# Performance work log

Measured on AMD Instinct MI355X. Metric: run time of the kernel, lower is better.

Reference implementation:

```python
import jax, jax.numpy as jnp
import numpy as np

N_NODES = 100000
N_EDGES = 1600000
IN_DIM, HID, N_CLS = 128, 256, 40


def setup_inputs() -> dict:
    key = jax.random.key(0)
    ks = jax.random.split(key, 8)
    x = jax.random.normal(ks[0], (N_NODES, IN_DIM), dtype=jnp.float32)
    edge_index = jax.random.randint(ks[1], (2, N_EDGES), 0, N_NODES, dtype=jnp.int64)
    def glorot(k, shape):
        scale = (6.0 / (shape[0] + shape[1])) ** 0.5
        return jax.random.uniform(k, shape, jnp.float32, -scale, scale)
    return {
        "x": x,
        "edge_index": edge_index,
        "W1": glorot(ks[2], (IN_DIM, HID)),
        "b1": jnp.zeros((HID,), jnp.float32),
        "W2": glorot(ks[3], (HID, HID)),
        "b2": jnp.zeros((HID,), jnp.float32),
        "W3": glorot(ks[4], (HID, N_CLS)),
        "b3": jnp.zeros((N_CLS,), jnp.float32),
    }


def _gcn_norm(edge_index, num_nodes):
    # Add self-loops, then symmetric normalization deg^-1/2 * deg^-1/2 (PyG GCNConv).
    loops = jnp.arange(num_nodes, dtype=edge_index.dtype)
    src = jnp.concatenate([edge_index[0], loops])
    dst = jnp.concatenate([edge_index[1], loops])
    deg = jax.ops.segment_sum(jnp.ones_like(dst, dtype=jnp.float32), dst,
                              num_segments=num_nodes)
    dinv = jnp.where(deg > 0, jax.lax.rsqrt(deg), 0.0)
    norm = dinv[src] * dinv[dst]  # [E + N]
    return src, dst, norm


def _gcn_conv(x, W, b, src, dst, norm, num_nodes):
    h = x @ W                       # [N, out] dense GEMM first (out <= in here is fine)
    msg = h[src] * norm[:, None]    # irregular gather, [E+N, out]
    out = jax.ops.segment_sum(msg, dst, num_segments=num_nodes)  # scatter-add
    return out + b


def reference(x, edge_index, W1, b1, W2, b2, W3, b3):
    n = x.shape[0]
    src, dst, norm = _gcn_norm(edge_index, n)
    h = jax.nn.relu(_gcn_conv(x, W1, b1, src, dst, norm, n))
    h = jax.nn.relu(_gcn_conv(h, W2, b2, src, dst, norm, n))
    h = _gcn_conv(h, W3, b3, src, dst, norm, n)
    return jax.nn.log_softmax(h, axis=1)
```

## Files before the change

kernel.cpp:

```cpp
#include <hip/hip_runtime.h>
#include <stdint.h>
#include <math.h>

#define N_NODES 100000
#define N_EDGES 1600000
#define IN_DIM 128
#define HID 256
#define N_CLS 40
#define NBKT 391
#define NPB 391

typedef __attribute__((ext_vector_type(8))) short short8;
typedef __attribute__((ext_vector_type(4))) float f32x4;

__device__ __forceinline__ unsigned short f2bf(float f) {
  unsigned b = __float_as_uint(f);
  b += 0x7fffu + ((b >> 16) & 1u);
  return (unsigned short)(b >> 16);
}
__device__ __forceinline__ float bflo(unsigned u) { return __uint_as_float(u << 16); }
__device__ __forceinline__ float bfhi(unsigned u) { return __uint_as_float(u & 0xffff0000u); }

__device__ __forceinline__ int load_idx(const void* eidx, int flag, size_t pos) {
  return flag ? (int)((const long long*)eidx)[pos] : ((const int*)eidx)[pos];
}

__global__ __launch_bounds__(512) void k_pre0(const unsigned int* __restrict__ ew,
                                              int* __restrict__ flag,
                                              int* __restrict__ hist) {
  int t = threadIdx.x;
  for (int k = t; k < NBKT; k += 512) hist[k] = 0;
  __shared__ unsigned int sh[512];
  unsigned int v = 0;
  for (int k = t; k < 4096; k += 512) v |= ew[2 * k + 1];
  sh[t] = v;
  __syncthreads();
  for (int s = 256; s > 0; s >>= 1) {
    if (t < s) sh[t] |= sh[t + s];
    __syncthreads();
  }
  if (t == 0) flag[0] = (sh[0] == 0u) ? 1 : 0;
}

__global__ __launch_bounds__(256) void k_hist(const void* __restrict__ eidx,
                                              const int* __restrict__ flagp,
                                              int* __restrict__ hist) {
  __shared__ int lh[NBKT];
  int t = threadIdx.x;
  for (int k = t; k < NBKT; k += 256) lh[k] = 0;
  __syncthreads();
  int flag = flagp[0];
  int base = blockIdx.x * 4096;
#pragma unroll
  for (int j = 0; j < 16; j++) {
    int e = base + j * 256 + t;
    if (e < N_EDGES) {
      int d = load_idx(eidx, flag, (size_t)N_EDGES + e);
      atomicAdd(&lh[d >> 8], 1);
    }
  }
  __syncthreads();
  for (int k = t; k < NBKT; k += 256) {
    int c = lh[k];
    if (c) atomicAdd(&hist[k], c);
  }
}

__global__ __launch_bounds__(512) void k_bscan(const int* __restrict__ hist,
                                               int* __restrict__ bucket_start,
                                               int* __restrict__ bucket_cursor) {
  __shared__ int sh[512];
  int t = threadIdx.x;
  int v = (t < NBKT) ? hist[t] : 0;
  sh[t] = v;
  __syncthreads();
  for (int off = 1; off < 512; off <<= 1) {
    int u = (t >= off) ? sh[t - off] : 0;
    __syncthreads();
    sh[t] += u;
    __syncthreads();
  }
  if (t < NBKT) {
    bucket_start[t + 1] = sh[t];
    bucket_cursor[t] = sh[t] - v;
  }
  if (t == 0) bucket_start[0] = 0;
}

__global__ __launch_bounds__(256) void k_part(const void* __restrict__ eidx,
                                              const int* __restrict__ flagp,
                                              int* __restrict__ bucket_cursor,
                                              uint2* __restrict__ bpairs) {
  __shared__ int lcur[NBKT];
  int t = threadIdx.x;
  for (int k = t; k < NBKT; k += 256) lcur[k] = 0;
  __syncthreads();
  int flag = flagp[0];
  int base = blockIdx.x * 4096;
#pragma unroll
  for (int j = 0; j < 16; j++) {
    int e = base + j * 256 + t;
    if (e < N_EDGES) {
      int d = load_idx(eidx, flag, (size_t)N_EDGES + e);
      atomicAdd(&lcur[d >> 8], 1);
    }
  }
  __syncthreads();
  for (int k = t; k < NBKT; k += 256) {
    int c = lcur[k];
    int g = c ? atomicAdd(&bucket_cursor[k], c) : 0;
    lcur[k] = g;
  }
  __syncthreads();
#pragma unroll
  for (int j = 0; j < 16; j++) {
    int e = base + j * 256 + t;
    if (e < N_EDGES) {
      int s = load_idx(eidx, flag, e);
      int d = load_idx(eidx, flag, (size_t)N_EDGES + e);
      int p = atomicAdd(&lcur[d >> 8], 1);
      bpairs[p] = make_uint2((unsigned)s, (unsigned)d);
    }
  }
}

__global__ __launch_bounds__(256) void k_bsort(const uint2* __restrict__ bpairs,
                                               const int* __restrict__ bucket_start,
                                               int* __restrict__ row_start,
                                               float* __restrict__ dinv,
                                               int* __restrict__ csr_src) {
  __shared__ int ldeg[256], lsum[256], lcur[256];
  int b = blockIdx.x, t = threadIdx.x;
  int d0 = b << 8;
  int nd = min(256, N_NODES - d0);
  int base = bucket_start[b];
  int n = bucket_start[b + 1] - base;
  ldeg[t] = 0;
  __syncthreads();
  for (int i = t; i < n; i += 256) {
    uint2 p = bpairs[base + i];
    atomicAdd(&ldeg[p.y - d0], 1);
  }
  __syncthreads();
  lsum[t] = ldeg[t];
  __syncthreads();
  for (int off = 1; off < 256; off <<= 1) {
    int v = (t >= off) ? lsum[t - off] : 0;
    __syncthreads();
    lsum[t] += v;
    __syncthreads();
  }
  int excl = lsum[t] - ldeg[t];
  if (t < nd) {
    row_start[d0 + t] = base + excl;
    dinv[d0 + t] = rsqrtf((float)(ldeg[t] + 1));
  }
  lcur[t] = base + excl;
  __syncthreads();
  for (int i = t; i < n; i += 256) {
    uint2 p = bpairs[base + i];
    int pos = atomicAdd(&lcur[p.y - d0], 1);
    csr_src[pos] = (int)p.x;
  }
  if (b == 0 && t == 0) row_start[N_NODES] = N_EDGES;
}

__global__ __launch_bounds__(256) void k_wprep(const float* __restrict__ W1,
                                               const float* __restrict__ W2,
                                               const float* __restrict__ W3,
                                               unsigned short* __restrict__ T1,
                                               unsigned short* __restrict__ T2,
                                               unsigned short* __restrict__ T3) {
  int idx = blockIdx.x * 256 + threadIdx.x;
  if (idx < 32768) {
    int n = idx >> 7, k = idx & 127;
    T1[idx] = f2bf(W1[(size_t)k * HID + n]);
  } else if (idx < 98304) {
    int j = idx - 32768;
    int n = j >> 8, k = j & 255;
    T2[j] = f2bf(W2[(size_t)k * HID + n]);
  } else if (idx < 131072) {
    int j = idx - 98304;
    int n = j >> 8, k = j & 255;
    T3[j] = f2bf((n < N_CLS) ? W3[(size_t)k * N_CLS + n] : 0.f);
  }
}

__global__ __launch_bounds__(256) void k_qx(const float* __restrict__ x,
                                            const float* __restrict__ dinv,
                                            unsigned short* __restrict__ xq,
                                            float* __restrict__ sw_x) {
  int node = (blockIdx.x << 2) + (threadIdx.x >> 6);
  int lane = threadIdx.x & 63;
  if (node >= N_NODES) return;
  float2 v = ((const float2*)x)[(size_t)node * 64 + lane];
  float m = fmaxf(fabsf(v.x), fabsf(v.y));
  for (int off = 32; off; off >>= 1) m = fmaxf(m, __shfl_down(m, off));
  m = __shfl(m, 0);
  float inv = (m > 0.f) ? 127.f / m : 0.f;
  int q0 = __float2int_rn(v.x * inv);
  int q1 = __float2int_rn(v.y * inv);
  xq[(size_t)node * 64 + lane] = (unsigned short)((q0 & 0xff) | ((q1 & 0xff) << 8));
  if (lane == 0) sw_x[node] = dinv[node] * ((m > 0.f) ? m / 127.f : 0.f);
}

__device__ __forceinline__ void up4u(unsigned v, float w,
                                     float& a0, float& a1, float& a2, float& a3) {
  a0 = fmaf((float)(v & 0xffu), w, a0);
  a1 = fmaf((float)((v >> 8) & 0xffu), w, a1);
  a2 = fmaf((float)((v >> 16) & 0xffu), w, a2);
  a3 = fmaf((float)(v >> 24), w, a3);
}

__global__ __launch_bounds__(256) void k_agg256i(const unsigned* __restrict__ tbl,
                                                 uint2* __restrict__ out,
                                                 const float* __restrict__ dinv,
                                                 const float* __restrict__ sw2,
                                                 const int* __restrict__ row_start,
                                                 const int* __restrict__ csr_src) {
  int node = (blockIdx.x << 2) + (threadIdx.x >> 6);
  int lane = threadIdx.x & 63;
  if (node >= N_NODES) return;
  const unsigned* col = tbl + lane;
  const float* sw = sw2 + ((lane >= 32) ? N_NODES : 0);
  float d = dinv[node];
  float ws = sw[node];
  unsigned v0 = col[(size_t)node * 64];
  float a0 = 0.f, a1 = 0.f, a2 = 0.f, a3 = 0.f;
  up4u(v0, ws, a0, a1, a2, a3);
  int e = row_start[node], e1 = row_start[node + 1];
  for (; e + 8 <= e1; e += 8) {
    int i0 = csr_src[e],     i1 = csr_src[e + 1], i2 = csr_src[e + 2], i3 = csr_src[e + 3];
    int i4 = csr_src[e + 4], i5 = csr_src[e + 5], i6 = csr_src[e + 6], i7 = csr_src[e + 7];
    float w0 = sw[i0], w1 = sw[i1], w2 = sw[i2], w3 = sw[i3];
    float w4 = sw[i4], w5 = sw[i5], w6 = sw[i6], w7 = sw[i7];
    unsigned r0 = col[(size_t)i0 * 64], r1 = col[(size_t)i1 * 64];
    unsigned r2 = col[(size_t)i2 * 64], r3 = col[(size_t)i3 * 64];
    unsigned r4 = col[(size_t)i4 * 64], r5 = col[(size_t)i5 * 64];
    unsigned r6 = col[(size_t)i6 * 64], r7 = col[(size_t)i7 * 64];
    up4u(r0, w0, a0, a1, a2, a3);
    up4u(r1, w1, a0, a1, a2, a3);
    up4u(r2, w2, a0, a1, a2, a3);
    up4u(r3, w3, a0, a1, a2, a3);
    up4u(r4, w4, a0, a1, a2, a3);
    up4u(r5, w5, a0, a1, a2, a3);
    up4u(r6, w6, a0, a1, a2, a3);
    up4u(r7, w7, a0, a1, a2, a3);
  }
  for (; e < e1; e++) {
    int i0 = csr_src[e];
    float w0 = sw[i0];
    unsigned r0 = col[(size_t)i0 * 64];
    up4u(r0, w0, a0, a1, a2, a3);
  }
  a0 *= d; a1 *= d; a2 *= d; a3 *= d;
  uint2 o;
  o.x = f2bf(a0) | ((unsigned)f2bf(a1) << 16);
  o.y = f2bf(a2) | ((unsigned)f2bf(a3) << 16);
  out[(size_t)node * 64 + lane] = o;
}

__global__ __launch_bounds__(256) void k_agg128i(const unsigned short* __restrict__ tbl,
                                                 unsigned* __restrict__ out,
                                                 const float* __restrict__ dinv,
                                                 const float* __restrict__ sw,
                                                 const int* __restrict__ row_start,
                                                 const int* __restrict__ csr_src) {
  int node = (blockIdx.x << 2) + (threadIdx.x >> 6);
  int lane = threadIdx.x & 63;
  if (node >= N_NODES) return;
  const unsigned short* col = tbl + lane;
  float d = dinv[node];
  float ws = sw[node];
  unsigned short v0 = col[(size_t)node * 64];
  float a0 = (float)(signed char)(v0 & 0xff) * ws;
  float a1 = (float)(signed char)(v0 >> 8) * ws;
  int e = row_start[node], e1 = row_start[node + 1];
  for (; e + 8 <= e1; e += 8) {
    int i0 = csr_src[e],     i1 = csr_src[e + 1], i2 = csr_src[e + 2], i3 = csr_src[e + 3];
    int i4 = csr_src[e + 4], i5 = csr_src[e + 5], i6 = csr_src[e + 6], i7 = csr_src[e + 7];
    float w0 = sw[i0], w1 = sw[i1], w2 = sw[i2], w3 = sw[i3];
    float w4 = sw[i4], w5 = sw[i5], w6 = sw[i6], w7 = sw[i7];
    unsigned short r0 = col[(size_t)i0 * 64], r1 = col[(size_t)i1 * 64];
    unsigned short r2 = col[(size_t)i2 * 64], r3 = col[(size_t)i3 * 64];
    unsigned short r4 = col[(size_t)i4 * 64], r5 = col[(size_t)i5 * 64];
    unsigned short r6 = col[(size_t)i6 * 64], r7 = col[(size_t)i7 * 64];
    a0 = fmaf((float)(signed char)(r0 & 0xff), w0, a0);
    a1 = fmaf((float)(signed char)(r0 >> 8), w0, a1);
    a0 = fmaf((float)(signed char)(r1 & 0xff), w1, a0);
    a1 = fmaf((float)(signed char)(r1 >> 8), w1, a1);
    a0 = fmaf((float)(signed char)(r2 & 0xff), w2, a0);
    a1 = fmaf((float)(signed char)(r2 >> 8), w2, a1);
    a0 = fmaf((float)(signed char)(r3 & 0xff), w3, a0);
    a1 = fmaf((float)(signed char)(r3 >> 8), w3, a1);
    a0 = fmaf((float)(signed char)(r4 & 0xff), w4, a0);
    a1 = fmaf((float)(signed char)(r4 >> 8), w4, a1);
    a0 = fmaf((float)(signed char)(r5 & 0xff), w5, a0);
    a1 = fmaf((float)(signed char)(r5 >> 8), w5, a1);
    a0 = fmaf((float)(signed char)(r6 & 0xff), w6, a0);
    a1 = fmaf((float)(signed char)(r6 >> 8), w6, a1);
    a0 = fmaf((float)(signed char)(r7 & 0xff), w7, a0);
    a1 = fmaf((float)(signed char)(r7 >> 8), w7, a1);
  }
  for (; e < e1; e++) {
    int i0 = csr_src[e];
    float w0 = sw[i0];
    unsigned short r0 = col[(size_t)i0 * 64];
    a0 = fmaf((float)(signed char)(r0 & 0xff), w0, a0);
    a1 = fmaf((float)(signed char)(r0 >> 8), w0, a1);
  }
  a0 *= d; a1 *= d;
  out[(size_t)node * 64 + lane] = f2bf(a0) | ((unsigned)f2bf(a1) << 16);
}

__global__ __launch_bounds__(256) void k_gemm_mfma(const unsigned short* __restrict__ A,
                                                   int lda,
                                                   const unsigned short* __restrict__ B,
                                                   const float* __restrict__ bias,
                                                   unsigned short* __restrict__ C, int ldc,
                                                   int M, int K, int relu) {
  __shared__ alignas(16) unsigned short As[128][40];
  __shared__ alignas(16) unsigned short Bs[128][40];
  int tid = threadIdx.x;
  int lane = tid & 63, wv = tid >> 6;
  int wy = wv >> 1, wx = wv & 1;
  int row0 = blockIdx.x * 128, col0 = blockIdx.y * 128;

  f32x4 acc[4][4];
#pragma unroll
  for (int i = 0; i < 4; i++)
#pragma unroll
    for (int j = 0; j < 4; j++) acc[i][j] = 0.f;

  int sr0 = tid >> 2;
  int sc = (tid & 3) * 8;

  for (int k0 = 0; k0 < K; k0 += 32) {
#pragma unroll
    for (int it = 0; it < 2; it++) {
      int r = sr0 + it * 64;
      int gr = row0 + r;
      short8 va = 0;
      if (gr < M) va = *(const short8*)(A + (size_t)gr * lda + k0 + sc);
      *(short8*)&As[r][sc] = va;
      short8 vb = *(const short8*)(B + (size_t)(col0 + r) * K + k0 + sc);
      *(short8*)&Bs[r][sc] = vb;
    }
    __syncthreads();

    int ar = wy * 64 + (lane & 15);
    int br = wx * 64 + (lane & 15);
    int kk = (lane >> 4) * 8;
    short8 a[4], b[4];
#pragma unroll
    for (int mi = 0; mi < 4; mi++) a[mi] = *(const short8*)&As[ar + mi * 16][kk];
#pragma unroll
    for (int ni = 0; ni < 4; ni++) b[ni] = *(const short8*)&Bs[br + ni * 16][kk];
#pragma unroll
    for (int mi = 0; mi < 4; mi++)
#pragma unroll
      for (int ni = 0; ni < 4; ni++)
        acc[mi][ni] = __builtin_amdgcn_mfma_f32_16x16x32_bf16(a[mi], b[ni], acc[mi][ni], 0, 0, 0);
    __syncthreads();
  }

  int mbase = row0 + wy * 64;
  int nbase = col0 + wx * 64;
#pragma unroll
  for (int ni = 0; ni < 4; ni++) {
    int gc = nbase + ni * 16 + (lane & 15);
    if (gc >= ldc) continue;
    float bz = bias ? bias[gc] : 0.f;
#pragma unroll
    for (int mi = 0; mi < 4; mi++) {
      f32x4 v = acc[mi][ni];
#pragma unroll
      for (int r = 0; r < 4; r++) {
        int gr = mbase + mi * 16 + (lane >> 4) * 4 + r;
        if (gr < M) {
          float o = v[r] + bz;
          if (relu) o = fmaxf(o, 0.f);
          C[(size_t)gr * ldc + gc] = f2bf(o);
        }
      }
    }
  }
}

__global__ __launch_bounds__(256) void k_gemm_q(const unsigned short* __restrict__ A,
                                                int lda,
                                                const unsigned short* __restrict__ B,
                                                const float* __restrict__ bias,
                                                const float* __restrict__ dinv,
                                                unsigned* __restrict__ hq,
                                                float* __restrict__ sw_h,
                                                int M, int K) {
  __shared__ alignas(16) unsigned short As[128][40];
  __shared__ alignas(16) unsigned short Bs[128][40];
  __shared__ float rmax[128][2];
  __shared__ float rscale[128];
  __shared__ alignas(16) unsigned char qtile[128][128];
  int tid = threadIdx.x;
  int lane = tid & 63, wv = tid >> 6;
  int wy = wv >> 1, wx = wv & 1;
  int quad = lane >> 4;
  int row0 = blockIdx.x * 128, col0 = blockIdx.y * 128;
  int half = blockIdx.y;

  f32x4 acc[4][4];
#pragma unroll
  for (int i = 0; i < 4; i++)
#pragma unroll
    for (int j = 0; j < 4; j++) acc[i][j] = 0.f;

  int sr0 = tid >> 2;
  int sc = (tid & 3) * 8;

  for (int k0 = 0; k0 < K; k0 += 32) {
#pragma unroll
    for (int it = 0; it < 2; it++) {
      int r = sr0 + it * 64;
      int gr = row0 + r;
      short8 va = 0;
      if (gr < M) va = *(const short8*)(A + (size_t)gr * lda + k0 + sc);
      *(short8*)&As[r][sc] = va;
      short8 vb = *(const short8*)(B + (size_t)(col0 + r) * K + k0 + sc);
      *(short8*)&Bs[r][sc] = vb;
    }
    __syncthreads();

    int ar = wy * 64 + (lane & 15);
    int br = wx * 64 + (lane & 15);
    int kk = quad * 8;
    short8 a[4], b[4];
#pragma unroll
    for (int mi = 0; mi < 4; mi++) a[mi] = *(const short8*)&As[ar + mi * 16][kk];
#pragma unroll
    for (int ni = 0; ni < 4; ni++) b[ni] = *(const short8*)&Bs[br + ni * 16][kk];
#pragma unroll
    for (int mi = 0; mi < 4; mi++)
#pragma unroll
      for (int ni = 0; ni < 4; ni++)
        acc[mi][ni] = __builtin_amdgcn_mfma_f32_16x16x32_bf16(a[mi], b[ni], acc[mi][ni], 0, 0, 0);
    __syncthreads();
  }

#pragma unroll
  for (int ni = 0; ni < 4; ni++) {
    int gc = col0 + wx * 64 + ni * 16 + (lane & 15);
    float bz = bias[gc];
#pragma unroll
    for (int mi = 0; mi < 4; mi++)
#pragma unroll
      for (int r = 0; r < 4; r++)
        acc[mi][ni][r] = fmaxf(acc[mi][ni][r] + bz, 0.f);
  }
  float m16[4][4];
#pragma unroll
  for (int mi = 0; mi < 4; mi++)
#pragma unroll
    for (int r = 0; r < 4; r++)
      m16[mi][r] = fmaxf(fmaxf(acc[mi][0][r], acc[mi][1][r]),
                         fmaxf(acc[mi][2][r], acc[mi][3][r]));
#pragma unroll
  for (int st = 1; st < 16; st <<= 1)
#pragma unroll
    for (int mi = 0; mi < 4; mi++)
#pragma unroll
      for (int r = 0; r < 4; r++)
        m16[mi][r] = fmaxf(m16[mi][r], __shfl_xor(m16[mi][r], st));
  {
    int i = lane & 15;
    int row = wy * 64 + (i >> 2) * 16 + quad * 4 + (i & 3);
    rmax[row][wx] = m16[i >> 2][i & 3];
  }
  __syncthreads();
  if (tid < 128) {
    float mx = fmaxf(rmax[tid][0], rmax[tid][1]);
    rscale[tid] = (mx > 0.f) ? 255.f / mx : 0.f;
    int grow = row0 + tid;
    if (grow < M) sw_h[half * N_NODES + grow] = dinv[grow] * ((mx > 0.f) ? mx / 255.f : 0.f);
  }
  __syncthreads();
#pragma unroll
  for (int ni = 0; ni < 4; ni++) {
    int c = wx * 64 + ni * 16 + (lane & 15);
#pragma unroll
    for (int mi = 0; mi < 4; mi++)
#pragma unroll
      for (int r = 0; r < 4; r++) {
        int row = wy * 64 + mi * 16 + quad * 4 + r;
        qtile[row][c] = (unsigned char)__float2uint_rn(acc[mi][ni][r] * rscale[row]);
      }
  }
  __syncthreads();
  const uint4* qt = (const uint4*)qtile;
#pragma unroll
  for (int k = 0; k < 4; k++) {
    int idx = tid + k * 256;
    int row = idx >> 3, p = idx & 7;
    int grow = row0 + row;
    if (grow < M)
      *(uint4*)(hq + (size_t)grow * 64 + half * 32 + p * 4) = qt[idx];
  }
}

__global__ __launch_bounds__(256) void k_agg40_lsm(const unsigned* __restrict__ in,
                                                   float* __restrict__ out,
                                                   const float* __restrict__ dinv,
                                                   const int* __restrict__ row_start,
                                                   const int* __restrict__ csr_src,
                                                   const float* __restrict__ bias) {
  int node = (blockIdx.x << 2) + (threadIdx.x >> 6);
  int lane = threadIdx.x & 63;
  if (node >= N_NODES) return;
  int g = (lane >= 40) ? 2 : (lane >= 20 ? 1 : 0);
  int c = lane - g * 20;
  bool act3 = lane < 60;
  const unsigned* base = in + c;
  float d = dinv[node];
  float ws = (g == 0 && act3) ? d : 0.f;
  unsigned u0 = base[(size_t)node * 32];
  float a0 = bflo(u0) * ws, a1 = bfhi(u0) * ws;
  int e1 = row_start[node + 1];
  int eb = row_start[node];
  for (; eb + 12 <= e1; eb += 12) {
    int ea = eb + g, eb2 = eb + 3 + g, ec = eb + 6 + g, ed = eb + 9 + g;
    int ia = csr_src[ea], ib = csr_src[eb2], ic = csr_src[ec], id = csr_src[ed];
    float wa = act3 ? dinv[ia] : 0.f;
    float wb = act3 ? dinv[ib] : 0.f;
    float wc = act3 ? dinv[ic] : 0.f;
    float wd = act3 ? dinv[id] : 0.f;
    unsigned ra = base[(size_t)ia * 32];
    unsigned rb = base[(size_t)ib * 32];
    unsigned rc = base[(size_t)ic * 32];
    unsigned rd = base[(size_t)id * 32];
    a0 = fmaf(bflo(ra), wa, a0); a1 = fmaf(bfhi(ra), wa, a1);
    a0 = fmaf(bflo(rb), wb, a0); a1 = fmaf(bfhi(rb), wb, a1);
    a0 = fmaf(bflo(rc), wc, a0); a1 = fmaf(bfhi(rc), wc, a1);
    a0 = fmaf(bflo(rd), wd, a0); a1 = fmaf(bfhi(rd), wd, a1);
  }
  for (; eb < e1; eb += 3) {
    int ea = eb + g;
    bool v = act3 && (ea < e1);
    int ia = v ? csr_src[ea] : 0;
    float wa = v ? dinv[ia] : 0.f;
    unsigned ra = base[(size_t)ia * 32];
    a0 = fmaf(bflo(ra), wa, a0); a1 = fmaf(bfhi(ra), wa, a1);
  }
  a0 += __shfl(a0, c + 20) + __shfl(a0, c + 40);
  a1 += __shfl(a1, c + 20) + __shfl(a1, c + 40);
  bool act = lane < 20;
  float v0 = act ? a0 * d + bias[2 * lane] : -INFINITY;
  float v1 = act ? a1 * d + bias[2 * lane + 1] : -INFINITY;
  float m = fmaxf(v0, v1);
  for (int off = 32; off; off >>= 1) m = fmaxf(m, __shfl_down(m, off));
  m = __shfl(m, 0);
  float s = act ? expf(v0 - m) + expf(v1 - m) : 0.f;
  for (int off = 32; off; off >>= 1) s += __shfl_down(s, off);
  s = __shfl(s, 0);
  float lse = m + logf(s);
  if (act) {
    out[(size_t)node * N_CLS + 2 * lane] = v0 - lse;
    out[(size_t)node * N_CLS + 2 * lane + 1] = v1 - lse;
  }
}

extern "C" void kernel_launch(void* const* d_in, const int* in_sizes, int n_in,
                              void* d_out, int out_size, void* d_ws, size_t ws_size,
                              hipStream_t stream) {
  const float* x  = (const float*)d_in[0];
  const void*  ei = d_in[1];
  const float* W1 = (const float*)d_in[2];
  const float* b1 = (const float*)d_in[3];
  const float* W2 = (const float*)d_in[4];
  const float* b2 = (const float*)d_in[5];
  const float* W3 = (const float*)d_in[6];
  const float* b3 = (const float*)d_in[7];
  float* out = (float*)d_out;

  char* w = (char*)d_ws;
  auto alloc = [&](size_t bytes) {
    char* p = w;
    w += (bytes + 255) & ~(size_t)255;
    return p;
  };
  int*   flag          = (int*)alloc(64);
  int*   hist          = (int*)alloc((size_t)NBKT * 4);
  int*   bucket_start  = (int*)alloc((size_t)(NBKT + 1) * 4);
  int*   bucket_cursor = (int*)alloc((size_t)NBKT * 4);
  uint2* bpairs        = (uint2*)alloc((size_t)N_EDGES * 8);
  int*   csr_src       = (int*)alloc((size_t)N_EDGES * 4);
  int*   row_start     = (int*)alloc(((size_t)N_NODES + 1) * 4);
  float* dinv          = (float*)alloc((size_t)N_NODES * 4);
  float* sw_x          = (float*)alloc((size_t)N_NODES * 4);
  float* sw_h          = (float*)alloc((size_t)N_NODES * 2 * 4);
  unsigned short* Wt1  = (unsigned short*)alloc((size_t)HID * IN_DIM * 2);
  unsigned short* Wt2  = (unsigned short*)alloc((size_t)HID * HID * 2);
  unsigned short* Wt3  = (unsigned short*)alloc((size_t)128 * HID * 2);
  unsigned short* xq   = (unsigned short*)alloc((size_t)N_NODES * 64 * 2);
  unsigned*       hq   = (unsigned*)alloc((size_t)N_NODES * 64 * 4);
  char* R0 = alloc((size_t)N_NODES * HID * 2);
  char* R1 = alloc((size_t)N_NODES * HID * 2);

  unsigned*       aggX  = (unsigned*)R0;
  uint2*          aggH1 = (uint2*)R0;
  unsigned short* h2    = (unsigned short*)R1;
  unsigned short* C3    = (unsigned short*)R0;

  const int nb_w1 = (N_NODES + 3) / 4;
  const int gm    = (N_NODES + 127) / 128;

  k_pre0<<<1, 512, 0, stream>>>((const unsigned int*)ei, flag, hist);
  k_hist<<<NPB, 256, 0, stream>>>(ei, flag, hist);
  k_bscan<<<1, 512, 0, stream>>>(hist, bucket_start, bucket_cursor);
  k_part<<<NPB, 256, 0, stream>>>(ei, flag, bucket_cursor, bpairs);
  k_bsort<<<NBKT, 256, 0, stream>>>(bpairs, bucket_start, row_start, dinv, csr_src);

  k_wprep<<<512, 256, 0, stream>>>(W1, W2, W3, Wt1, Wt2, Wt3);
  k_qx<<<nb_w1, 256, 0, stream>>>(x, dinv, xq, sw_x);

  k_agg128i<<<nb_w1, 256, 0, stream>>>(xq, aggX, dinv, sw_x, row_start, csr_src);
  k_gemm_q<<<dim3(gm, 2), 256, 0, stream>>>((const unsigned short*)aggX, IN_DIM, Wt1, b1,
                                            dinv, hq, sw_h, N_NODES, IN_DIM);
  k_agg256i<<<nb_w1, 256, 0, stream>>>(hq, aggH1, dinv, sw_h, row_start, csr_src);
  k_gemm_mfma<<<dim3(gm, 2), 256, 0, stream>>>((const unsigned short*)aggH1, HID, Wt2, b2,
                                               h2, HID, N_NODES, HID, 1);
  k_gemm_mfma<<<dim3(gm, 1), 256, 0, stream>>>(h2, HID, Wt3, nullptr,
                                               C3, 64, N_NODES, HID, 0);
  k_agg40_lsm<<<nb_w1, 256, 0, stream>>>((const unsigned*)C3, out, dinv, row_start,
                                         csr_src, b3);
}
```

Measured before the change: 525.0 us.

## Prefetch scalarized CSR indices and interleave per-half scale weights in aggregation kernels

Both aggregation kernels now make node and row bounds wave-uniform with readfirstlane. Each loads the next eight neighbor indices as scalars one iteration ahead, and handles the remainder with a padded masked batch of eight instead of a scalar tail loop. The per-node scale array for the 256-wide layer is stored interleaved (node*2+half) instead of as two separate halves, so both halves of a wave read adjacent words. The aim is to cut vector index loads, overlap index fetch with gathers, and improve locality of weight reads. In exchange the tail always issues eight gathers, some redundant, and the GEMM epilogue's store layout changes to match.

```diff
diff --git a/kernel.cpp b/kernel.cpp
--- a/kernel.cpp
+++ b/kernel.cpp
@@ -215,44 +215,64 @@
 __global__ __launch_bounds__(256) void k_agg256i(const unsigned* __restrict__ tbl,
                                                  uint2* __restrict__ out,
                                                  const float* __restrict__ dinv,
-                                                 const float* __restrict__ sw2,
+                                                 const float* __restrict__ swp,
                                                  const int* __restrict__ row_start,
                                                  const int* __restrict__ csr_src) {
   int node = (blockIdx.x << 2) + (threadIdx.x >> 6);
   int lane = threadIdx.x & 63;
   if (node >= N_NODES) return;
+  node = __builtin_amdgcn_readfirstlane(node);
+  int hoff = (lane >= 32) ? 1 : 0;
   const unsigned* col = tbl + lane;
-  const float* sw = sw2 + ((lane >= 32) ? N_NODES : 0);
   float d = dinv[node];
-  float ws = sw[node];
+  float ws = swp[2 * node + hoff];
   unsigned v0 = col[(size_t)node * 64];
   float a0 = 0.f, a1 = 0.f, a2 = 0.f, a3 = 0.f;
   up4u(v0, ws, a0, a1, a2, a3);
-  int e = row_start[node], e1 = row_start[node + 1];
-  for (; e + 8 <= e1; e += 8) {
-    int i0 = csr_src[e],     i1 = csr_src[e + 1], i2 = csr_src[e + 2], i3 = csr_src[e + 3];
-    int i4 = csr_src[e + 4], i5 = csr_src[e + 5], i6 = csr_src[e + 6], i7 = csr_src[e + 7];
-    float w0 = sw[i0], w1 = sw[i1], w2 = sw[i2], w3 = sw[i3];
-    float w4 = sw[i4], w5 = sw[i5], w6 = sw[i6], w7 = sw[i7];
-    unsigned r0 = col[(size_t)i0 * 64], r1 = col[(size_t)i1 * 64];
-    unsigned r2 = col[(size_t)i2 * 64], r3 = col[(size_t)i3 * 64];
-    unsigned r4 = col[(size_t)i4 * 64], r5 = col[(size_t)i5 * 64];
-    unsigned r6 = col[(size_t)i6 * 64], r7 = col[(size_t)i7 * 64];
-    up4u(r0, w0, a0, a1, a2, a3);
-    up4u(r1, w1, a0, a1, a2, a3);
-    up4u(r2, w2, a0, a1, a2, a3);
-    up4u(r3, w3, a0, a1, a2, a3);
-    up4u(r4, w4, a0, a1, a2, a3);
-    up4u(r5, w5, a0, a1, a2, a3);
-    up4u(r6, w6, a0, a1, a2, a3);
-    up4u(r7, w7, a0, a1, a2, a3);
-  }
-  for (; e < e1; e++) {
-    int i0 = csr_src[e];
-    float w0 = sw[i0];
-    unsigned r0 = col[(size_t)i0 * 64];
-    up4u(r0, w0, a0, a1, a2, a3);
-  }
+
+  int e0 = __builtin_amdgcn_readfirstlane(row_start[node]);
+  int e1 = __builtin_amdgcn_readfirstlane(row_start[node + 1]);
+  const int* ep = csr_src + e0;
+  int n = e1 - e0;
+
+  int idx[8];
+  if (n > 0) {
+#pragma unroll
+    for (int j = 0; j < 8; j++) idx[j] = __builtin_amdgcn_readfirstlane(ep[min(j, n - 1)]);
+  }
+  int k = 0;
+  for (; k + 8 <= n; k += 8) {
+    int cur[8];
+#pragma unroll
+    for (int j = 0; j < 8; j++) cur[j] = idx[j];
+    if (k + 8 < n) {
+#pragma unroll
+      for (int j = 0; j < 8; j++)
+        idx[j] = __builtin_amdgcn_readfirstlane(ep[min(k + 8 + j, n - 1)]);
+    }
+    unsigned r[8];
+    float w[8];
+#pragma unroll
+    for (int j = 0; j < 8; j++) r[j] = col[(size_t)cur[j] * 64];
+#pragma unroll
+    for (int j = 0; j < 8; j++) w[j] = swp[2 * cur[j] + hoff];
+#pragma unroll
+    for (int j = 0; j < 8; j++) up4u(r[j], w[j], a0, a1, a2, a3);
+  }
+  if (k < n) {
+    unsigned r[8];
+    float w[8];
+#pragma unroll
+    for (int j = 0; j < 8; j++) r[j] = col[(size_t)idx[j] * 64];
+#pragma unroll
+    for (int j = 0; j < 8; j++) {
+      float wv = swp[2 * idx[j] + hoff];
+      w[j] = (k + j < n) ? wv : 0.f;
+    }
+#pragma unroll
+    for (int j = 0; j < 8; j++) up4u(r[j], w[j], a0, a1, a2, a3);
+  }
+
   a0 *= d; a1 *= d; a2 *= d; a3 *= d;
   uint2 o;
   o.x = f2bf(a0) | ((unsigned)f2bf(a1) << 16);
@@ -269,46 +289,63 @@
   int node = (blockIdx.x << 2) + (threadIdx.x >> 6);
   int lane = threadIdx.x & 63;
   if (node >= N_NODES) return;
+  node = __builtin_amdgcn_readfirstlane(node);
   const unsigned short* col = tbl + lane;
   float d = dinv[node];
   float ws = sw[node];
   unsigned short v0 = col[(size_t)node * 64];
   float a0 = (float)(signed char)(v0 & 0xff) * ws;
   float a1 = (float)(signed char)(v0 >> 8) * ws;
-  int e = row_start[node], e1 = row_start[node + 1];
-  for (; e + 8 <= e1; e += 8) {
-    int i0 = csr_src[e],     i1 = csr_src[e + 1], i2 = csr_src[e + 2], i3 = csr_src[e + 3];
-    int i4 = csr_src[e + 4], i5 = csr_src[e + 5], i6 = csr_src[e + 6], i7 = csr_src[e + 7];
-    float w0 = sw[i0], w1 = sw[i1], w2 = sw[i2], w3 = sw[i3];
-    float w4 = sw[i4], w5 = sw[i5], w6 = sw[i6], w7 = sw[i7];
-    unsigned short r0 = col[(size_t)i0 * 64], r1 = col[(size_t)i1 * 64];
-    unsigned short r2 = col[(size_t)i2 * 64], r3 = col[(size_t)i3 * 64];
-    unsigned short r4 = col[(size_t)i4 * 64], r5 = col[(size_t)i5 * 64];
-    unsigned short r6 = col[(size_t)i6 * 64], r7 = col[(size_t)i7 * 64];
-    a0 = fmaf((float)(signed char)(r0 & 0xff), w0, a0);
-    a1 = fmaf((float)(signed char)(r0 >> 8), w0, a1);
-    a0 = fmaf((float)(signed char)(r1 & 0xff), w1, a0);
-    a1 = fmaf((float)(signed char)(r1 >> 8), w1, a1);
-    a0 = fmaf((float)(signed char)(r2 & 0xff), w2, a0);
-    a1 = fmaf((float)(signed char)(r2 >> 8), w2, a1);
-    a0 = fmaf((float)(signed char)(r3 & 0xff), w3, a0);
-    a1 = fmaf((float)(signed char)(r3 >> 8), w3, a1);
-    a0 = fmaf((float)(signed char)(r4 & 0xff), w4, a0);
-    a1 = fmaf((float)(signed char)(r4 >> 8), w4, a1);
-    a0 = fmaf((float)(signed char)(r5 & 0xff), w5, a0);
-    a1 = fmaf((float)(signed char)(r5 >> 8), w5, a1);
-    a0 = fmaf((float)(signed char)(r6 & 0xff), w6, a0);
-    a1 = fmaf((float)(signed char)(r6 >> 8), w6, a1);
-    a0 = fmaf((float)(signed char)(r7 & 0xff), w7, a0);
-    a1 = fmaf((float)(signed char)(r7 >> 8), w7, a1);
-  }
-  for (; e < e1; e++) {
-    int i0 = csr_src[e];
-    float w0 = sw[i0];
-    unsigned short r0 = col[(size_t)i0 * 64];
-    a0 = fmaf((float)(signed char)(r0 & 0xff), w0, a0);
-    a1 = fmaf((float)(signed char)(r0 >> 8), w0, a1);
-  }
+
+  int e0 = __builtin_amdgcn_readfirstlane(row_start[node]);
+  int e1 = __builtin_amdgcn_readfirstlane(row_start[node + 1]);
+  const int* ep = csr_src + e0;
+  int n = e1 - e0;
+
+  int idx[8];
+  if (n > 0) {
+#pragma unroll
+    for (int j = 0; j < 8; j++) idx[j] = __builtin_amdgcn_readfirstlane(ep[min(j, n - 1)]);
+  }
+  int k = 0;
+  for (; k + 8 <= n; k += 8) {
+    int cur[8];
+#pragma unroll
+    for (int j = 0; j < 8; j++) cur[j] = idx[j];
+    if (k + 8 < n) {
+#pragma unroll
+      for (int j = 0; j < 8; j++)
+        idx[j] = __builtin_amdgcn_readfirstlane(ep[min(k + 8 + j, n - 1)]);
+    }
+    unsigned short r[8];
+    float w[8];
+#pragma unroll
+    for (int j = 0; j < 8; j++) r[j] = col[(size_t)cur[j] * 64];
+#pragma unroll
+    for (int j = 0; j < 8; j++) w[j] = sw[cur[j]];
+#pragma unroll
+    for (int j = 0; j < 8; j++) {
+      a0 = fmaf((float)(signed char)(r[j] & 0xff), w[j], a0);
+      a1 = fmaf((float)(signed char)(r[j] >> 8), w[j], a1);
+    }
+  }
+  if (k < n) {
+    unsigned short r[8];
+    float w[8];
+#pragma unroll
+    for (int j = 0; j < 8; j++) r[j] = col[(size_t)idx[j] * 64];
+#pragma unroll
+    for (int j = 0; j < 8; j++) {
+      float wv = sw[idx[j]];
+      w[j] = (k + j < n) ? wv : 0.f;
+    }
+#pragma unroll
+    for (int j = 0; j < 8; j++) {
+      a0 = fmaf((float)(signed char)(r[j] & 0xff), w[j], a0);
+      a1 = fmaf((float)(signed char)(r[j] >> 8), w[j], a1);
+    }
+  }
+
   a0 *= d; a1 *= d;
   out[(size_t)node * 64 + lane] = f2bf(a0) | ((unsigned)f2bf(a1) << 16);
 }
@@ -479,7 +516,7 @@
     float mx = fmaxf(rmax[tid][0], rmax[tid][1]);
     rscale[tid] = (mx > 0.f) ? 255.f / mx : 0.f;
     int grow = row0 + tid;
-    if (grow < M) sw_h[half * N_NODES + grow] = dinv[grow] * ((mx > 0.f) ? mx / 255.f : 0.f);
+    if (grow < M) sw_h[(size_t)grow * 2 + half] = dinv[grow] * ((mx > 0.f) ? mx / 255.f : 0.f);
   }
   __syncthreads();
 #pragma unroll
```

Measured after the change: 507.0 us. -3.4%, faster.
